# Optimization experiments

Hardware: AMD Instinct MI355X
Metric: run time of the kernel (lower is better)

## Reference

```python
import jax, jax.numpy as jnp
import numpy as np

N, E, D, G = 50000, 600000, 128, 1024
NEG_SLOPE = 0.2  # PyG GATConv default negative_slope


def setup_inputs() -> dict:
    key = jax.random.key(0)
    ks = jax.random.split(key, 20)
    s = 1.0 / np.sqrt(D)
    inp = {
        "x": jax.random.normal(ks[0], (N, D), jnp.float32),
        "edge_index": jax.random.randint(ks[1], (2, E), 0, N, dtype=jnp.int64),
        "edge_attr": jax.random.normal(ks[2], (E, 1), jnp.float32),  # ignored (edge_dim=None)
        "batch": jnp.sort(jax.random.randint(ks[3], (N,), 0, G, dtype=jnp.int64)),
    }
    k = 4
    for name in ("g1", "g2", "g3"):
        inp[f"{name}_W"] = jax.random.normal(ks[k], (D, D), jnp.float32) * s; k += 1
        inp[f"{name}_a_src"] = jax.random.normal(ks[k], (D,), jnp.float32) * s; k += 1
        inp[f"{name}_a_dst"] = jax.random.normal(ks[k], (D,), jnp.float32) * s; k += 1
        inp[f"{name}_b"] = jnp.zeros((D,), jnp.float32)
    inp["lin_W"] = jax.random.normal(ks[k], (D, D), jnp.float32) * s
    inp["lin_b"] = jnp.zeros((D,), jnp.float32)
    return inp


def _gat(x, src, dst, W, a_src, a_dst, b):
    # PyG GATConv, heads=1: project, edge attention logits, scatter-softmax over
    # destination nodes, weighted scatter-add aggregation, plus bias.
    n = x.shape[0]
    h = x @ W                                            # [N, D]
    logits = jax.nn.leaky_relu((h @ a_src)[src] + (h @ a_dst)[dst], NEG_SLOPE)  # [E']
    m = jax.ops.segment_max(logits, dst, num_segments=n)
    p = jnp.exp(logits - m[dst])
    denom = jax.ops.segment_sum(p, dst, num_segments=n)
    alpha = p / (denom[dst] + 1e-16)                     # PyG softmax eps
    out = jax.ops.segment_sum(alpha[:, None] * h[src], dst, num_segments=n)
    return out + b


def reference(x, edge_index, edge_attr, batch,
              g1_W, g1_a_src, g1_a_dst, g1_b,
              g2_W, g2_a_src, g2_a_dst, g2_b,
              g3_W, g3_a_src, g3_a_dst, g3_b,
              lin_W, lin_b):
    n = x.shape[0]
    # GATConv default add_self_loops=True
    loop = jnp.arange(n, dtype=edge_index.dtype)
    src = jnp.concatenate([edge_index[0], loop])
    dst = jnp.concatenate([edge_index[1], loop])

    h = jax.nn.relu(_gat(x, src, dst, g1_W, g1_a_src, g1_a_dst, g1_b))
    h = jax.nn.relu(_gat(h, src, dst, g2_W, g2_a_src, g2_a_dst, g2_b))
    h = _gat(h, src, dst, g3_W, g3_a_src, g3_a_dst, g3_b)

    # global_mean_pool over graph ids
    sums = jax.ops.segment_sum(h, batch, num_segments=G)
    cnts = jax.ops.segment_sum(jnp.ones((n,), h.dtype), batch, num_segments=G)
    pooled = sums / jnp.maximum(cnts, 1.0)[:, None]
    # dropout(p=0.5) is identity in eval mode
    return pooled @ lin_W + lin_b
```

## Files before the change

### kernel.cpp

```cpp
#include <hip/hip_runtime.h>

#define D 128
typedef unsigned short ushort_t;
typedef __attribute__((ext_vector_type(8))) short bf16x8;
typedef __attribute__((ext_vector_type(4))) float f32x4;

__device__ __forceinline__ float wred_max(float v){
#pragma unroll
  for (int o = 1; o < 64; o <<= 1) v = fmaxf(v, __shfl_xor(v, o, 64));
  return v;
}
__device__ __forceinline__ float wred_sum(float v){
#pragma unroll
  for (int o = 1; o < 64; o <<= 1) v += __shfl_xor(v, o, 64);
  return v;
}
__device__ __forceinline__ unsigned short f2bf(float f){
  unsigned u = __float_as_uint(f);
  unsigned r = (u + 0x7FFFu + ((u >> 16) & 1u)) >> 16;
  return (unsigned short)r;
}
__device__ __forceinline__ float bflo(unsigned u){ return __uint_as_float(u << 16); }
__device__ __forceinline__ float bfhi(unsigned u){ return __uint_as_float(u & 0xFFFF0000u); }

__global__ __launch_bounds__(256) void k_init(const float* __restrict__ W0,
                                              const float* __restrict__ W1,
                                              const float* __restrict__ W2,
                                              ushort_t* __restrict__ Wp,
                                              int* __restrict__ cnt, int n){
  int b = blockIdx.x;
  if (b < 192){
    int wi = b >> 6;
    const float* W = wi == 0 ? W0 : (wi == 1 ? W1 : W2);
    ushort_t* dst = Wp + wi * 16384;
    int idx = (b & 63) * 256 + threadIdx.x;
    int k = idx >> 7, c = idx & 127;
    int ct = c >> 4, s = k >> 5, lane = (c & 15) | (((k >> 3) & 3) << 4), e = k & 7;
    dst[((ct * 4 + s) * 64 + lane) * 8 + e] = f2bf(W[idx]);
  } else {
    int i = (b - 192) * 256 + threadIdx.x;
    if (i < n) cnt[i] = 0;
  }
}

template<bool XF32>
__device__ __forceinline__ void gemm_body(int bid, const void* __restrict__ Av,
                                          const ushort_t* __restrict__ Wp,
                                          const float* __restrict__ a_src,
                                          const float* __restrict__ a_dst,
                                          ushort_t* __restrict__ Hbf,
                                          float* __restrict__ as_,
                                          float* __restrict__ ad_,
                                          int n){
  int tid = threadIdx.x;
  int wid = tid >> 6, l = tid & 63;
  int kg = l >> 4, cin = l & 15;
  int r0 = bid * 64 + wid * 16;
  int row_l = r0 + cin;
  if (row_l > n - 1) row_l = n - 1;

  bf16x8 ah[4];
  if (XF32){
    const float* xp = (const float*)Av + (size_t)row_l * D + kg * 8;
#pragma unroll
    for (int s = 0; s < 4; s++){
      float4 f0 = *(const float4*)(xp + s * 32);
      float4 f1 = *(const float4*)(xp + s * 32 + 4);
      ah[s][0] = (short)f2bf(f0.x); ah[s][1] = (short)f2bf(f0.y);
      ah[s][2] = (short)f2bf(f0.z); ah[s][3] = (short)f2bf(f0.w);
      ah[s][4] = (short)f2bf(f1.x); ah[s][5] = (short)f2bf(f1.y);
      ah[s][6] = (short)f2bf(f1.z); ah[s][7] = (short)f2bf(f1.w);
    }
  } else {
    const ushort_t* xp = (const ushort_t*)Av + (size_t)row_l * D + kg * 8;
#pragma unroll
    for (int s = 0; s < 4; s++) ah[s] = *(const bf16x8*)(xp + s * 32);
  }

  const bf16x8* Bh = (const bf16x8*)Wp;

  f32x4 acc[8];
#pragma unroll
  for (int ct = 0; ct < 8; ct++) acc[ct] = (f32x4){0.f, 0.f, 0.f, 0.f};

#pragma unroll
  for (int ct = 0; ct < 8; ct++)
#pragma unroll
    for (int s = 0; s < 4; s++)
      acc[ct] = __builtin_amdgcn_mfma_f32_16x16x32_bf16(ah[s], Bh[(ct * 4 + s) * 64 + l], acc[ct], 0, 0, 0);

  float asv[8], adv[8];
#pragma unroll
  for (int ct = 0; ct < 8; ct++){
    asv[ct] = a_src[ct * 16 + cin];
    adv[ct] = a_dst[ct * 16 + cin];
  }
#pragma unroll
  for (int j = 0; j < 4; j++){
    float ps = 0.f, pd = 0.f;
#pragma unroll
    for (int ct = 0; ct < 8; ct++){ ps += acc[ct][j] * asv[ct]; pd += acc[ct][j] * adv[ct]; }
#pragma unroll
    for (int o = 1; o < 16; o <<= 1){ ps += __shfl_xor(ps, o, 64); pd += __shfl_xor(pd, o, 64); }
    int row = r0 + kg * 4 + j;
    if (row < n){
      if (cin == 0) as_[row] = ps;
      if (cin == 1) ad_[row] = pd;
#pragma unroll
      for (int ct = 0; ct < 8; ct++)
        Hbf[(size_t)row * D + ct * 16 + cin] = f2bf(acc[ct][j]);
    }
  }
}

__global__ __launch_bounds__(256) void k_gemm_mfma_bf(const void* __restrict__ Av,
                                                      const ushort_t* __restrict__ Wp,
                                                      const float* __restrict__ a_src,
                                                      const float* __restrict__ a_dst,
                                                      ushort_t* __restrict__ Hbf,
                                                      float* __restrict__ as_,
                                                      float* __restrict__ ad_,
                                                      int n){
  gemm_body<false>(blockIdx.x, Av, Wp, a_src, a_dst, Hbf, as_, ad_, n);
}

__global__ __launch_bounds__(256) void k_gemm1_fill(const float* __restrict__ x,
                                                    const ushort_t* __restrict__ Wp,
                                                    const float* __restrict__ a_src,
                                                    const float* __restrict__ a_dst,
                                                    ushort_t* __restrict__ Hbf,
                                                    float* __restrict__ as_,
                                                    float* __restrict__ ad_,
                                                    int n, int gemm_grid,
                                                    const int* __restrict__ src,
                                                    const int* __restrict__ dst,
                                                    int E, int EP,
                                                    int* __restrict__ cnt,
                                                    ushort_t* __restrict__ csr_pad){
  int b = blockIdx.x;
  if (b < gemm_grid){
    gemm_body<true>(b, x, Wp, a_src, a_dst, Hbf, as_, ad_, n);
  } else {
    int e = (b - gemm_grid) * 256 + threadIdx.x;
    if (e >= EP) return;
    int s, d;
    if (e < E){ s = src[e]; d = dst[e]; } else { s = d = e - E; }
    int slot = atomicAdd(&cnt[d], 1);
    if (slot < 64) csr_pad[((size_t)d << 6) + slot] = (ushort_t)s;
  }
}

template<bool OUTBF>
__global__ __launch_bounds__(256) void k_agg(const uint4* __restrict__ hb4,
                                             const ushort_t* __restrict__ csr_pad,
                                             const int* __restrict__ cnt,
                                             const float* __restrict__ asrc,
                                             const float* __restrict__ adst,
                                             const float* __restrict__ bias,
                                             ushort_t* __restrict__ outb,
                                             float* __restrict__ outf,
                                             int relu, int n){
  int node = (blockIdx.x * 256 + threadIdx.x) >> 6;
  if (node >= n) return;
  int lane = threadIdx.x & 63;
  int q = lane & 15, g = lane >> 4;
  int deg = cnt[node]; if (deg > 64) deg = 64;
  const ushort_t* eb = csr_pad + ((size_t)node << 6);
  float adn = adst[node];

  int s = 0; float logit = -1e30f;
  if (lane < deg){
    s = eb[lane];
    float xx = asrc[s] + adn;
    logit = xx >= 0.f ? xx : 0.2f * xx;
  }
  float m = wred_max(logit);
  float p = (lane < deg) ? __expf(logit - m) : 0.f;
  float denom = wred_sum(p);
  float inv = 1.f / (denom + 1e-16f);

  float acc[8] = {0.f, 0.f, 0.f, 0.f, 0.f, 0.f, 0.f, 0.f};
#pragma unroll 2
  for (int j = 0; j < deg; j += 4){
    int slot = j + g;
    int   sj = __shfl(s, slot, 64);
    float wj = (slot < deg) ? __shfl(p, slot, 64) : 0.f;
    uint4 v = hb4[(size_t)sj * 16 + q];
    acc[0] += wj * bflo(v.x); acc[1] += wj * bfhi(v.x);
    acc[2] += wj * bflo(v.y); acc[3] += wj * bfhi(v.y);
    acc[4] += wj * bflo(v.z); acc[5] += wj * bfhi(v.z);
    acc[6] += wj * bflo(v.w); acc[7] += wj * bfhi(v.w);
  }

#pragma unroll
  for (int o = 16; o < 64; o <<= 1){
#pragma unroll
    for (int i = 0; i < 8; i++) acc[i] += __shfl_xor(acc[i], o, 64);
  }

  if (g == 0){
    float4 b0 = *(const float4*)&bias[q * 8];
    float4 b1 = *(const float4*)&bias[q * 8 + 4];
    float o0 = acc[0] * inv + b0.x, o1 = acc[1] * inv + b0.y;
    float o2 = acc[2] * inv + b0.z, o3 = acc[3] * inv + b0.w;
    float o4 = acc[4] * inv + b1.x, o5 = acc[5] * inv + b1.y;
    float o6 = acc[6] * inv + b1.z, o7 = acc[7] * inv + b1.w;
    if (relu){
      o0 = fmaxf(o0, 0.f); o1 = fmaxf(o1, 0.f); o2 = fmaxf(o2, 0.f); o3 = fmaxf(o3, 0.f);
      o4 = fmaxf(o4, 0.f); o5 = fmaxf(o5, 0.f); o6 = fmaxf(o6, 0.f); o7 = fmaxf(o7, 0.f);
    }
    if (OUTBF){
      ushort4 u0, u1;
      u0.x = f2bf(o0); u0.y = f2bf(o1); u0.z = f2bf(o2); u0.w = f2bf(o3);
      u1.x = f2bf(o4); u1.y = f2bf(o5); u1.z = f2bf(o6); u1.w = f2bf(o7);
      *(ushort4*)&outb[(size_t)node * D + q * 8]     = u0;
      *(ushort4*)&outb[(size_t)node * D + q * 8 + 4] = u1;
    } else {
      *(float4*)&outf[(size_t)node * D + q * 8]     = make_float4(o0, o1, o2, o3);
      *(float4*)&outf[(size_t)node * D + q * 8 + 4] = make_float4(o4, o5, o6, o7);
    }
  }
}

__device__ __forceinline__ int lbound(const int* a, int n, int key){
  int lo = 0, hi = n;
  while (lo < hi){ int mid = (lo + hi) >> 1; if (a[mid] < key) lo = mid + 1; else hi = mid; }
  return lo;
}

__global__ __launch_bounds__(128) void k_pool_final(const float* __restrict__ x,
                                                    const int* __restrict__ batch,
                                                    const float* __restrict__ Wl,
                                                    const float* __restrict__ bl,
                                                    float* __restrict__ out, int n){
  __shared__ float pl[128];
  int g = blockIdx.x;
  int c = threadIdx.x;
  int lo = lbound(batch, n, g);
  int hi = lbound(batch, n, g + 1);
  float sum = 0.f;
  for (int i = lo; i < hi; i++) sum += x[(size_t)i * D + c];
  float cnt = (float)(hi - lo);
  pl[c] = sum / fmaxf(cnt, 1.f);
  __syncthreads();
  float acc = bl[c];
#pragma unroll 4
  for (int k = 0; k < 128; k++) acc += pl[k] * Wl[(size_t)k * D + c];
  out[(size_t)g * D + c] = acc;
}

extern "C" void kernel_launch(void* const* d_in, const int* in_sizes, int n_in,
                              void* d_out, int out_size, void* d_ws, size_t ws_size,
                              hipStream_t stream){
  const float* x     = (const float*)d_in[0];
  const int*   ei    = (const int*)d_in[1];
  const int*   batch = (const int*)d_in[3];
  const float* gW[3]  = {(const float*)d_in[4],  (const float*)d_in[8],  (const float*)d_in[12]};
  const float* gAs[3] = {(const float*)d_in[5],  (const float*)d_in[9],  (const float*)d_in[13]};
  const float* gAd[3] = {(const float*)d_in[6],  (const float*)d_in[10], (const float*)d_in[14]};
  const float* gB[3]  = {(const float*)d_in[7],  (const float*)d_in[11], (const float*)d_in[15]};
  const float* linW = (const float*)d_in[16];
  const float* linB = (const float*)d_in[17];
  float* outp = (float*)d_out;

  int N  = in_sizes[3];
  int E  = in_sizes[1] / 2;
  int EP = E + N;
  int G  = out_size / D;

  char* ws = (char*)d_ws;
  size_t off = 0;
  auto alloc = [&](size_t bytes)->void*{
    void* p = ws + off;
    off += (bytes + 255) & ~(size_t)255;
    return p;
  };
  float*    bufF    = (float*)alloc((size_t)N * D * 4);
  ushort_t* bufB    = (ushort_t*)alloc((size_t)N * D * 2);
  ushort_t* Hbf     = (ushort_t*)alloc((size_t)N * D * 2);
  float*    as_     = (float*)alloc((size_t)N * 4);
  float*    ad_     = (float*)alloc((size_t)N * 4);
  int*      cnt     = (int*)  alloc((size_t)N * 4);
  ushort_t* csr_pad = (ushort_t*)alloc((size_t)N * 64 * 2);
  ushort_t* Wp      = (ushort_t*)alloc(3 * 16384 * 2);
  (void)ws_size; (void)n_in;

  const int* esrc = ei;
  const int* edst = ei + E;

  int tpb = 256;
  int egrid = (EP + tpb - 1) / tpb;
  int ngrid = (N + tpb - 1) / tpb;
  int gemm_grid = (N + 63) / 64;
  int node_grid = (N + 3) / 4;

  k_init<<<192 + ngrid, tpb, 0, stream>>>(gW[0], gW[1], gW[2], Wp, cnt, N);

  const uint4* hbu = (const uint4*)Hbf;

  k_gemm1_fill<<<gemm_grid + egrid, tpb, 0, stream>>>(x, Wp, gAs[0], gAd[0], Hbf, as_, ad_, N,
                                                      gemm_grid, esrc, edst, E, EP, cnt, csr_pad);
  k_agg<true>  <<<node_grid, tpb, 0, stream>>>(hbu, csr_pad, cnt, as_, ad_, gB[0], bufB, nullptr, 1, N);
  k_gemm_mfma_bf<<<gemm_grid, tpb, 0, stream>>>(bufB, Wp + 16384, gAs[1], gAd[1], Hbf, as_, ad_, N);
  k_agg<true>  <<<node_grid, tpb, 0, stream>>>(hbu, csr_pad, cnt, as_, ad_, gB[1], bufB, nullptr, 1, N);
  k_gemm_mfma_bf<<<gemm_grid, tpb, 0, stream>>>(bufB, Wp + 32768, gAs[2], gAd[2], Hbf, as_, ad_, N);
  k_agg<false> <<<node_grid, tpb, 0, stream>>>(hbu, csr_pad, cnt, as_, ad_, gB[2], nullptr, bufF, 0, N);

  k_pool_final<<<G, 128, 0, stream>>>(bufF, batch, linW, linB, outp, N);
}
```

Measured before the change: 216.1 us.

## Fuse all GAT stages into one cooperative persistent kernel with grid syncs

Replaces the eight separate kernel launches with a single cooperative persistent kernel that walks each stage in grid-stride loops, separated by grid.sync. The goal is to remove launch gaps and tail effects between stages. It also splits the weights into bf16 hi/lo halves and issues two MFMAs per step for better accuracy, which doubles GEMM MFMA work. Self loops are now handled implicitly in the aggregation instead of being inserted into the CSR. Pooling uses 256 threads per graph. The added host-side property and occupancy queries on every call, plus the grid-wide barriers, add their own overhead.

```diff
diff --git a/kernel.cpp b/kernel.cpp
--- a/kernel.cpp
+++ b/kernel.cpp
@@ -1,10 +1,22 @@
 #include <hip/hip_runtime.h>
+#include <hip/hip_cooperative_groups.h>
+
+namespace cg = cooperative_groups;
 
 #define D 128
 typedef unsigned short ushort_t;
 typedef __attribute__((ext_vector_type(8))) short bf16x8;
 typedef __attribute__((ext_vector_type(4))) float f32x4;
 
+struct MegaP {
+  const float* x; const int* esrc; const int* edst; const int* batch;
+  const float* W[3]; const float* As[3]; const float* Ad[3]; const float* Bb[3];
+  const float* linW; const float* linB; float* out;
+  float* bufF; ushort_t* bufB; ushort_t* Hbf; float* nsrc; float* ndst;
+  int* cnt; ushort_t* csr; ushort_t* Wp;
+  int N, E, G;
+};
+
 __device__ __forceinline__ float wred_max(float v){
 #pragma unroll
   for (int o = 1; o < 64; o <<= 1) v = fmaxf(v, __shfl_xor(v, o, 64));
@@ -22,39 +34,48 @@
 }
 __device__ __forceinline__ float bflo(unsigned u){ return __uint_as_float(u << 16); }
 __device__ __forceinline__ float bfhi(unsigned u){ return __uint_as_float(u & 0xFFFF0000u); }
-
-__global__ __launch_bounds__(256) void k_init(const float* __restrict__ W0,
-                                              const float* __restrict__ W1,
-                                              const float* __restrict__ W2,
-                                              ushort_t* __restrict__ Wp,
-                                              int* __restrict__ cnt, int n){
-  int b = blockIdx.x;
+__device__ __forceinline__ int lbound(const int* a, int n, int key){
+  int lo = 0, hi = n;
+  while (lo < hi){ int mid = (lo + hi) >> 1; if (a[mid] < key) lo = mid + 1; else hi = mid; }
+  return lo;
+}
+
+__device__ __forceinline__ void init_body(int b, const MegaP& p){
   if (b < 192){
     int wi = b >> 6;
-    const float* W = wi == 0 ? W0 : (wi == 1 ? W1 : W2);
-    ushort_t* dst = Wp + wi * 16384;
+    const float* W = p.W[wi];
+    ushort_t* dst = p.Wp + wi * 32768;
     int idx = (b & 63) * 256 + threadIdx.x;
     int k = idx >> 7, c = idx & 127;
+    float w = W[idx];
+    unsigned short hi = f2bf(w);
+    float r = w - __uint_as_float((unsigned)hi << 16);
     int ct = c >> 4, s = k >> 5, lane = (c & 15) | (((k >> 3) & 3) << 4), e = k & 7;
-    dst[((ct * 4 + s) * 64 + lane) * 8 + e] = f2bf(W[idx]);
+    int off = ((ct * 4 + s) * 64 + lane) * 8 + e;
+    dst[off] = hi;
+    dst[16384 + off] = f2bf(r);
   } else {
     int i = (b - 192) * 256 + threadIdx.x;
-    if (i < n) cnt[i] = 0;
-  }
+    if (i < p.N) p.cnt[i] = 0;
+  }
+}
+
+__device__ __forceinline__ void fill_body(int vb, const MegaP& p){
+  int e = vb * 256 + (int)threadIdx.x;
+  if (e >= p.E) return;
+  int s = p.esrc[e], d = p.edst[e];
+  int slot = atomicAdd(&p.cnt[d], 1);
+  if (slot < 63) p.csr[((size_t)d << 6) + slot] = (ushort_t)s;
 }
 
 template<bool XF32>
-__device__ __forceinline__ void gemm_body(int bid, const void* __restrict__ Av,
-                                          const ushort_t* __restrict__ Wp,
-                                          const float* __restrict__ a_src,
-                                          const float* __restrict__ a_dst,
-                                          ushort_t* __restrict__ Hbf,
-                                          float* __restrict__ as_,
-                                          float* __restrict__ ad_,
-                                          int n){
-  int tid = threadIdx.x;
+__device__ __forceinline__ void gemm_body(int bid, const void* Av, const ushort_t* Wp,
+                                          const float* a_src, const float* a_dst,
+                                          const MegaP& p){
+  int tid = (int)threadIdx.x;
   int wid = tid >> 6, l = tid & 63;
   int kg = l >> 4, cin = l & 15;
+  int n = p.N;
   int r0 = bid * 64 + wid * 16;
   int row_l = r0 + cin;
   if (row_l > n - 1) row_l = n - 1;
@@ -78,6 +99,7 @@
   }
 
   const bf16x8* Bh = (const bf16x8*)Wp;
+  const bf16x8* Bl = (const bf16x8*)(Wp + 16384);
 
   f32x4 acc[8];
 #pragma unroll
@@ -86,8 +108,10 @@
 #pragma unroll
   for (int ct = 0; ct < 8; ct++)
 #pragma unroll
-    for (int s = 0; s < 4; s++)
+    for (int s = 0; s < 4; s++){
       acc[ct] = __builtin_amdgcn_mfma_f32_16x16x32_bf16(ah[s], Bh[(ct * 4 + s) * 64 + l], acc[ct], 0, 0, 0);
+      acc[ct] = __builtin_amdgcn_mfma_f32_16x16x32_bf16(ah[s], Bl[(ct * 4 + s) * 64 + l], acc[ct], 0, 0, 0);
+    }
 
   float asv[8], adv[8];
 #pragma unroll
@@ -104,94 +128,52 @@
     for (int o = 1; o < 16; o <<= 1){ ps += __shfl_xor(ps, o, 64); pd += __shfl_xor(pd, o, 64); }
     int row = r0 + kg * 4 + j;
     if (row < n){
-      if (cin == 0) as_[row] = ps;
-      if (cin == 1) ad_[row] = pd;
+      if (cin == 0) p.nsrc[row] = ps;
+      if (cin == 1) p.ndst[row] = pd;
 #pragma unroll
       for (int ct = 0; ct < 8; ct++)
-        Hbf[(size_t)row * D + ct * 16 + cin] = f2bf(acc[ct][j]);
-    }
-  }
-}
-
-__global__ __launch_bounds__(256) void k_gemm_mfma_bf(const void* __restrict__ Av,
-                                                      const ushort_t* __restrict__ Wp,
-                                                      const float* __restrict__ a_src,
-                                                      const float* __restrict__ a_dst,
-                                                      ushort_t* __restrict__ Hbf,
-                                                      float* __restrict__ as_,
-                                                      float* __restrict__ ad_,
-                                                      int n){
-  gemm_body<false>(blockIdx.x, Av, Wp, a_src, a_dst, Hbf, as_, ad_, n);
-}
-
-__global__ __launch_bounds__(256) void k_gemm1_fill(const float* __restrict__ x,
-                                                    const ushort_t* __restrict__ Wp,
-                                                    const float* __restrict__ a_src,
-                                                    const float* __restrict__ a_dst,
-                                                    ushort_t* __restrict__ Hbf,
-                                                    float* __restrict__ as_,
-                                                    float* __restrict__ ad_,
-                                                    int n, int gemm_grid,
-                                                    const int* __restrict__ src,
-                                                    const int* __restrict__ dst,
-                                                    int E, int EP,
-                                                    int* __restrict__ cnt,
-                                                    ushort_t* __restrict__ csr_pad){
-  int b = blockIdx.x;
-  if (b < gemm_grid){
-    gemm_body<true>(b, x, Wp, a_src, a_dst, Hbf, as_, ad_, n);
-  } else {
-    int e = (b - gemm_grid) * 256 + threadIdx.x;
-    if (e >= EP) return;
-    int s, d;
-    if (e < E){ s = src[e]; d = dst[e]; } else { s = d = e - E; }
-    int slot = atomicAdd(&cnt[d], 1);
-    if (slot < 64) csr_pad[((size_t)d << 6) + slot] = (ushort_t)s;
+        p.Hbf[(size_t)row * D + ct * 16 + cin] = f2bf(acc[ct][j]);
+    }
   }
 }
 
 template<bool OUTBF>
-__global__ __launch_bounds__(256) void k_agg(const uint4* __restrict__ hb4,
-                                             const ushort_t* __restrict__ csr_pad,
-                                             const int* __restrict__ cnt,
-                                             const float* __restrict__ asrc,
-                                             const float* __restrict__ adst,
-                                             const float* __restrict__ bias,
-                                             ushort_t* __restrict__ outb,
-                                             float* __restrict__ outf,
-                                             int relu, int n){
-  int node = (blockIdx.x * 256 + threadIdx.x) >> 6;
-  if (node >= n) return;
-  int lane = threadIdx.x & 63;
+__device__ __forceinline__ void agg_body(int vb, const float* bias,
+                                         ushort_t* outb, float* outf, bool relu,
+                                         const MegaP& p){
+  int node = (vb * 256 + (int)threadIdx.x) >> 6;
+  if (node >= p.N) return;
+  int lane = (int)threadIdx.x & 63;
   int q = lane & 15, g = lane >> 4;
-  int deg = cnt[node]; if (deg > 64) deg = 64;
-  const ushort_t* eb = csr_pad + ((size_t)node << 6);
-  float adn = adst[node];
-
-  int s = 0; float logit = -1e30f;
-  if (lane < deg){
-    s = eb[lane];
-    float xx = asrc[s] + adn;
+  int degr = p.cnt[node]; if (degr > 63) degr = 63;
+  int degp = degr + 1;
+  const ushort_t* eb = p.csr + ((size_t)node << 6);
+  float adn = p.ndst[node];
+
+  int s = node; float logit = -1e30f;
+  if (lane < degr) s = eb[lane];
+  if (lane <= degr){
+    float xx = p.nsrc[s] + adn;
     logit = xx >= 0.f ? xx : 0.2f * xx;
   }
   float m = wred_max(logit);
-  float p = (lane < deg) ? __expf(logit - m) : 0.f;
-  float denom = wred_sum(p);
+  float pp = (lane <= degr) ? __expf(logit - m) : 0.f;
+  float denom = wred_sum(pp);
   float inv = 1.f / (denom + 1e-16f);
 
+  const uint4* hb4 = (const uint4*)p.Hbf;
   float acc[8] = {0.f, 0.f, 0.f, 0.f, 0.f, 0.f, 0.f, 0.f};
 #pragma unroll 2
-  for (int j = 0; j < deg; j += 4){
+  for (int j = 0; j < degp; j += 4){
     int slot = j + g;
     int   sj = __shfl(s, slot, 64);
-    float wj = (slot < deg) ? __shfl(p, slot, 64) : 0.f;
+    float wj = (slot < degp) ? __shfl(pp, slot, 64) : 0.f;
     uint4 v = hb4[(size_t)sj * 16 + q];
     acc[0] += wj * bflo(v.x); acc[1] += wj * bfhi(v.x);
     acc[2] += wj * bflo(v.y); acc[3] += wj * bfhi(v.y);
     acc[4] += wj * bflo(v.z); acc[5] += wj * bfhi(v.z);
     acc[6] += wj * bflo(v.w); acc[7] += wj * bfhi(v.w);
   }
-
 #pragma unroll
   for (int o = 16; o < 64; o <<= 1){
 #pragma unroll
@@ -222,50 +204,70 @@
   }
 }
 
-__device__ __forceinline__ int lbound(const int* a, int n, int key){
-  int lo = 0, hi = n;
-  while (lo < hi){ int mid = (lo + hi) >> 1; if (a[mid] < key) lo = mid + 1; else hi = mid; }
-  return lo;
-}
-
-__global__ __launch_bounds__(128) void k_pool_final(const float* __restrict__ x,
-                                                    const int* __restrict__ batch,
-                                                    const float* __restrict__ Wl,
-                                                    const float* __restrict__ bl,
-                                                    float* __restrict__ out, int n){
+__device__ __forceinline__ void pool_body(int gid, const MegaP& p){
+  __shared__ float part[2][128];
   __shared__ float pl[128];
-  int g = blockIdx.x;
-  int c = threadIdx.x;
-  int lo = lbound(batch, n, g);
-  int hi = lbound(batch, n, g + 1);
+  int tid = (int)threadIdx.x;
+  int c = tid & 127, h2 = tid >> 7;
+  int lo = lbound(p.batch, p.N, gid);
+  int hi = lbound(p.batch, p.N, gid + 1);
   float sum = 0.f;
-  for (int i = lo; i < hi; i++) sum += x[(size_t)i * D + c];
-  float cnt = (float)(hi - lo);
-  pl[c] = sum / fmaxf(cnt, 1.f);
+  for (int i = lo + h2; i < hi; i += 2) sum += p.bufF[(size_t)i * D + c];
+  part[h2][c] = sum;
   __syncthreads();
-  float acc = bl[c];
+  if (h2 == 0){
+    float cf = (float)(hi - lo);
+    pl[c] = (part[0][c] + part[1][c]) / fmaxf(cf, 1.f);
+  }
+  __syncthreads();
+  float acc = 0.f;
+  int k0 = h2 * 64;
 #pragma unroll 4
-  for (int k = 0; k < 128; k++) acc += pl[k] * Wl[(size_t)k * D + c];
-  out[(size_t)g * D + c] = acc;
+  for (int k = k0; k < k0 + 64; k++) acc += pl[k] * p.linW[(size_t)k * D + c];
+  part[h2][c] = acc;
+  __syncthreads();
+  if (h2 == 0) p.out[(size_t)gid * D + c] = part[0][c] + part[1][c] + p.linB[c];
+  __syncthreads();
+}
+
+__global__ __launch_bounds__(256, 4) void k_mega(MegaP p){
+  cg::grid_group grid = cg::this_grid();
+  int nb = (int)gridDim.x;
+  int ngrid = (p.N + 255) >> 8;
+  int egrid = (p.E + 255) >> 8;
+  int gemm_grid = (p.N + 63) >> 6;
+  int node_grid = (p.N + 3) >> 2;
+
+  for (int b = (int)blockIdx.x; b < 192 + ngrid; b += nb) init_body(b, p);
+  grid.sync();
+  for (int b = (int)blockIdx.x; b < gemm_grid + egrid; b += nb){
+    if (b < gemm_grid) gemm_body<true>(b, p.x, p.Wp, p.As[0], p.Ad[0], p);
+    else fill_body(b - gemm_grid, p);
+  }
+  grid.sync();
+  for (int b = (int)blockIdx.x; b < node_grid; b += nb)
+    agg_body<true>(b, p.Bb[0], p.bufB, nullptr, true, p);
+  grid.sync();
+  for (int b = (int)blockIdx.x; b < gemm_grid; b += nb)
+    gemm_body<false>(b, p.bufB, p.Wp + 32768, p.As[1], p.Ad[1], p);
+  grid.sync();
+  for (int b = (int)blockIdx.x; b < node_grid; b += nb)
+    agg_body<true>(b, p.Bb[1], p.bufB, nullptr, true, p);
+  grid.sync();
+  for (int b = (int)blockIdx.x; b < gemm_grid; b += nb)
+    gemm_body<false>(b, p.bufB, p.Wp + 65536, p.As[2], p.Ad[2], p);
+  grid.sync();
+  for (int b = (int)blockIdx.x; b < node_grid; b += nb)
+    agg_body<false>(b, p.Bb[2], nullptr, p.bufF, false, p);
+  grid.sync();
+  for (int b = (int)blockIdx.x; b < p.G; b += nb) pool_body(b, p);
 }
 
 extern "C" void kernel_launch(void* const* d_in, const int* in_sizes, int n_in,
                               void* d_out, int out_size, void* d_ws, size_t ws_size,
                               hipStream_t stream){
-  const float* x     = (const float*)d_in[0];
-  const int*   ei    = (const int*)d_in[1];
-  const int*   batch = (const int*)d_in[3];
-  const float* gW[3]  = {(const float*)d_in[4],  (const float*)d_in[8],  (const float*)d_in[12]};
-  const float* gAs[3] = {(const float*)d_in[5],  (const float*)d_in[9],  (const float*)d_in[13]};
-  const float* gAd[3] = {(const float*)d_in[6],  (const float*)d_in[10], (const float*)d_in[14]};
-  const float* gB[3]  = {(const float*)d_in[7],  (const float*)d_in[11], (const float*)d_in[15]};
-  const float* linW = (const float*)d_in[16];
-  const float* linB = (const float*)d_in[17];
-  float* outp = (float*)d_out;
-
   int N  = in_sizes[3];
   int E  = in_sizes[1] / 2;
-  int EP = E + N;
   int G  = out_size / D;
 
   char* ws = (char*)d_ws;
@@ -275,36 +277,44 @@
     off += (bytes + 255) & ~(size_t)255;
     return p;
   };
-  float*    bufF    = (float*)alloc((size_t)N * D * 4);
-  ushort_t* bufB    = (ushort_t*)alloc((size_t)N * D * 2);
-  ushort_t* Hbf     = (ushort_t*)alloc((size_t)N * D * 2);
-  float*    as_     = (float*)alloc((size_t)N * 4);
-  float*    ad_     = (float*)alloc((size_t)N * 4);
-  int*      cnt     = (int*)  alloc((size_t)N * 4);
-  ushort_t* csr_pad = (ushort_t*)alloc((size_t)N * 64 * 2);
-  ushort_t* Wp      = (ushort_t*)alloc(3 * 16384 * 2);
+
+  MegaP p;
+  p.x     = (const float*)d_in[0];
+  p.esrc  = (const int*)d_in[1];
+  p.edst  = (const int*)d_in[1] + E;
+  p.batch = (const int*)d_in[3];
+  for (int i = 0; i < 3; i++){
+    p.W[i]  = (const float*)d_in[4 + i * 4];
+    p.As[i] = (const float*)d_in[5 + i * 4];
+    p.Ad[i] = (const float*)d_in[6 + i * 4];
+    p.Bb[i] = (const float*)d_in[7 + i * 4];
+  }
+  p.linW = (const float*)d_in[16];
+  p.linB = (const float*)d_in[17];
+  p.out  = (float*)d_out;
+
+  p.bufF = (float*)alloc((size_t)N * D * 4);
+  p.bufB = (ushort_t*)alloc((size_t)N * D * 2);
+  p.Hbf  = (ushort_t*)alloc((size_t)N * D * 2);
+  p.nsrc = (float*)alloc((size_t)N * 4);
+  p.ndst = (float*)alloc((size_t)N * 4);
+  p.cnt  = (int*)alloc((size_t)N * 4);
+  p.csr  = (ushort_t*)alloc((size_t)N * 64 * 2);
+  p.Wp   = (ushort_t*)alloc(3 * 2 * 16384 * 2);
+  p.N = N; p.E = E; p.G = G;
   (void)ws_size; (void)n_in;
 
-  const int* esrc = ei;
-  const int* edst = ei + E;
-
-  int tpb = 256;
-  int egrid = (EP + tpb - 1) / tpb;
-  int ngrid = (N + tpb - 1) / tpb;
-  int gemm_grid = (N + 63) / 64;
-  int node_grid = (N + 3) / 4;
-
-  k_init<<<192 + ngrid, tpb, 0, stream>>>(gW[0], gW[1], gW[2], Wp, cnt, N);
-
-  const uint4* hbu = (const uint4*)Hbf;
-
-  k_gemm1_fill<<<gemm_grid + egrid, tpb, 0, stream>>>(x, Wp, gAs[0], gAd[0], Hbf, as_, ad_, N,
-                                                      gemm_grid, esrc, edst, E, EP, cnt, csr_pad);
-  k_agg<true>  <<<node_grid, tpb, 0, stream>>>(hbu, csr_pad, cnt, as_, ad_, gB[0], bufB, nullptr, 1, N);
-  k_gemm_mfma_bf<<<gemm_grid, tpb, 0, stream>>>(bufB, Wp + 16384, gAs[1], gAd[1], Hbf, as_, ad_, N);
-  k_agg<true>  <<<node_grid, tpb, 0, stream>>>(hbu, csr_pad, cnt, as_, ad_, gB[1], bufB, nullptr, 1, N);
-  k_gemm_mfma_bf<<<gemm_grid, tpb, 0, stream>>>(bufB, Wp + 32768, gAs[2], gAd[2], Hbf, as_, ad_, N);
-  k_agg<false> <<<node_grid, tpb, 0, stream>>>(hbu, csr_pad, cnt, as_, ad_, gB[2], nullptr, bufF, 0, N);
-
-  k_pool_final<<<G, 128, 0, stream>>>(bufF, batch, linW, linB, outp, N);
-}
+  int dev = 0;
+  hipGetDevice(&dev);
+  hipDeviceProp_t prop;
+  hipGetDeviceProperties(&prop, dev);
+  int bpc = 0;
+  hipOccupancyMaxActiveBlocksPerMultiprocessor(&bpc, k_mega, 256, 0);
+  if (bpc < 1) bpc = 1;
+  long long grid = (long long)bpc * prop.multiProcessorCount;
+  if (grid > 2048) grid = 2048;
+
+  void* kargs[] = { (void*)&p };
+  hipLaunchCooperativeKernel((const void*)k_mega, dim3((unsigned)grid), dim3(256),
+                             kargs, 0, stream);
+}
```

Result: slower. 835.6 us (+286.6%).

## Split weights into bf16 hi/lo pair and synthesize self-loops in aggregation

Applied to the files above, without the earlier changes.

Weights are stored as a bf16 high part plus a bf16 residual, and each GEMM issues two MFMAs per step for better accuracy. The self-loop edges are no longer scattered through atomics into the padded CSR. The aggregation kernel adds the node itself as an implicit extra neighbor, with the stored degree capped at 63. This removes N atomic inserts from the fill phase but doubles the MFMA work and the weight loads in all three GEMMs.

```diff
diff --git a/kernel.cpp b/kernel.cpp
--- a/kernel.cpp
+++ b/kernel.cpp
@@ -32,11 +32,16 @@
   if (b < 192){
     int wi = b >> 6;
     const float* W = wi == 0 ? W0 : (wi == 1 ? W1 : W2);
-    ushort_t* dst = Wp + wi * 16384;
+    ushort_t* dst = Wp + wi * 32768;
     int idx = (b & 63) * 256 + threadIdx.x;
     int k = idx >> 7, c = idx & 127;
+    float w = W[idx];
+    unsigned short hi = f2bf(w);
+    float r = w - __uint_as_float((unsigned)hi << 16);
     int ct = c >> 4, s = k >> 5, lane = (c & 15) | (((k >> 3) & 3) << 4), e = k & 7;
-    dst[((ct * 4 + s) * 64 + lane) * 8 + e] = f2bf(W[idx]);
+    int off = ((ct * 4 + s) * 64 + lane) * 8 + e;
+    dst[off] = hi;
+    dst[16384 + off] = f2bf(r);
   } else {
     int i = (b - 192) * 256 + threadIdx.x;
     if (i < n) cnt[i] = 0;
@@ -78,6 +83,7 @@
   }
 
   const bf16x8* Bh = (const bf16x8*)Wp;
+  const bf16x8* Bl = (const bf16x8*)(Wp + 16384);
 
   f32x4 acc[8];
 #pragma unroll
@@ -86,8 +92,10 @@
 #pragma unroll
   for (int ct = 0; ct < 8; ct++)
 #pragma unroll
-    for (int s = 0; s < 4; s++)
+    for (int s = 0; s < 4; s++){
       acc[ct] = __builtin_amdgcn_mfma_f32_16x16x32_bf16(ah[s], Bh[(ct * 4 + s) * 64 + l], acc[ct], 0, 0, 0);
+      acc[ct] = __builtin_amdgcn_mfma_f32_16x16x32_bf16(ah[s], Bl[(ct * 4 + s) * 64 + l], acc[ct], 0, 0, 0);
+    }
 
   float asv[8], adv[8];
 #pragma unroll
@@ -134,7 +142,7 @@
                                                     int n, int gemm_grid,
                                                     const int* __restrict__ src,
                                                     const int* __restrict__ dst,
-                                                    int E, int EP,
+                                                    int E,
                                                     int* __restrict__ cnt,
                                                     ushort_t* __restrict__ csr_pad){
   int b = blockIdx.x;
@@ -142,11 +150,10 @@
     gemm_body<true>(b, x, Wp, a_src, a_dst, Hbf, as_, ad_, n);
   } else {
     int e = (b - gemm_grid) * 256 + threadIdx.x;
-    if (e >= EP) return;
-    int s, d;
-    if (e < E){ s = src[e]; d = dst[e]; } else { s = d = e - E; }
+    if (e >= E) return;
+    int s = src[e], d = dst[e];
     int slot = atomicAdd(&cnt[d], 1);
-    if (slot < 64) csr_pad[((size_t)d << 6) + slot] = (ushort_t)s;
+    if (slot < 63) csr_pad[((size_t)d << 6) + slot] = (ushort_t)s;
   }
 }
 
@@ -164,27 +171,28 @@
   if (node >= n) return;
   int lane = threadIdx.x & 63;
   int q = lane & 15, g = lane >> 4;
-  int deg = cnt[node]; if (deg > 64) deg = 64;
+  int degr = cnt[node]; if (degr > 63) degr = 63;
+  int degp = degr + 1;
   const ushort_t* eb = csr_pad + ((size_t)node << 6);
   float adn = adst[node];
 
-  int s = 0; float logit = -1e30f;
-  if (lane < deg){
-    s = eb[lane];
+  int s = node; float logit = -1e30f;
+  if (lane < degr) s = eb[lane];
+  if (lane <= degr){
     float xx = asrc[s] + adn;
     logit = xx >= 0.f ? xx : 0.2f * xx;
   }
   float m = wred_max(logit);
-  float p = (lane < deg) ? __expf(logit - m) : 0.f;
+  float p = (lane <= degr) ? __expf(logit - m) : 0.f;
   float denom = wred_sum(p);
   float inv = 1.f / (denom + 1e-16f);
 
   float acc[8] = {0.f, 0.f, 0.f, 0.f, 0.f, 0.f, 0.f, 0.f};
 #pragma unroll 2
-  for (int j = 0; j < deg; j += 4){
+  for (int j = 0; j < degp; j += 4){
     int slot = j + g;
     int   sj = __shfl(s, slot, 64);
-    float wj = (slot < deg) ? __shfl(p, slot, 64) : 0.f;
+    float wj = (slot < degp) ? __shfl(p, slot, 64) : 0.f;
     uint4 v = hb4[(size_t)sj * 16 + q];
     acc[0] += wj * bflo(v.x); acc[1] += wj * bfhi(v.x);
     acc[2] += wj * bflo(v.y); acc[3] += wj * bfhi(v.y);
@@ -265,7 +273,6 @@
 
   int N  = in_sizes[3];
   int E  = in_sizes[1] / 2;
-  int EP = E + N;
   int G  = out_size / D;
 
   char* ws = (char*)d_ws;
@@ -282,14 +289,14 @@
   float*    ad_     = (float*)alloc((size_t)N * 4);
   int*      cnt     = (int*)  alloc((size_t)N * 4);
   ushort_t* csr_pad = (ushort_t*)alloc((size_t)N * 64 * 2);
-  ushort_t* Wp      = (ushort_t*)alloc(3 * 16384 * 2);
+  ushort_t* Wp      = (ushort_t*)alloc(3 * 2 * 16384 * 2);
   (void)ws_size; (void)n_in;
 
   const int* esrc = ei;
   const int* edst = ei + E;
 
   int tpb = 256;
-  int egrid = (EP + tpb - 1) / tpb;
+  int egrid = (E + tpb - 1) / tpb;
   int ngrid = (N + tpb - 1) / tpb;
   int gemm_grid = (N + 63) / 64;
   int node_grid = (N + 3) / 4;
@@ -299,11 +306,11 @@
   const uint4* hbu = (const uint4*)Hbf;
 
   k_gemm1_fill<<<gemm_grid + egrid, tpb, 0, stream>>>(x, Wp, gAs[0], gAd[0], Hbf, as_, ad_, N,
-                                                      gemm_grid, esrc, edst, E, EP, cnt, csr_pad);
+                                                      gemm_grid, esrc, edst, E, cnt, csr_pad);
   k_agg<true>  <<<node_grid, tpb, 0, stream>>>(hbu, csr_pad, cnt, as_, ad_, gB[0], bufB, nullptr, 1, N);
-  k_gemm_mfma_bf<<<gemm_grid, tpb, 0, stream>>>(bufB, Wp + 16384, gAs[1], gAd[1], Hbf, as_, ad_, N);
+  k_gemm_mfma_bf<<<gemm_grid, tpb, 0, stream>>>(bufB, Wp + 32768, gAs[1], gAd[1], Hbf, as_, ad_, N);
   k_agg<true>  <<<node_grid, tpb, 0, stream>>>(hbu, csr_pad, cnt, as_, ad_, gB[1], bufB, nullptr, 1, N);
-  k_gemm_mfma_bf<<<gemm_grid, tpb, 0, stream>>>(bufB, Wp + 32768, gAs[2], gAd[2], Hbf, as_, ad_, N);
+  k_gemm_mfma_bf<<<gemm_grid, tpb, 0, stream>>>(bufB, Wp + 65536, gAs[2], gAd[2], Hbf, as_, ad_, N);
   k_agg<false> <<<node_grid, tpb, 0, stream>>>(hbu, csr_pad, cnt, as_, ad_, gB[2], nullptr, bufF, 0, N);
 
   k_pool_final<<<G, 128, 0, stream>>>(bufF, batch, linW, linB, outp, N);
```

New measurement: 227.3 us. +5.2%, slower.
